# Optimization experiments

Measured on AMD Instinct MI355X. Metric: run time of the kernel, lower is better.

Reference implementation:

```python
import jax, jax.numpy as jnp
import numpy as np

SPATIAL_SHAPES = [(128, 128), (64, 64), (32, 32), (16, 16)]
B, Q, D, NH, NL, NP = 8, 900, 256, 8, 4, 4
S = sum(h * w for h, w in SPATIAL_SHAPES)  # 21760
HD = D // NH


def bilinear_sample(img, x, y):
    # img: (H, W, C); x, y: (Q, P) pixel coords (grid_sample align_corners=False convention)
    H, W, _ = img.shape
    x0 = jnp.floor(x)
    y0 = jnp.floor(y)
    out = 0.0
    for yi in (y0, y0 + 1.0):
        for xi in (x0, x0 + 1.0):
            w = (1.0 - jnp.abs(x - xi)) * (1.0 - jnp.abs(y - yi))
            valid = (xi >= 0) & (xi <= W - 1) & (yi >= 0) & (yi <= H - 1)
            xc = jnp.clip(xi, 0, W - 1).astype(jnp.int32)
            yc = jnp.clip(yi, 0, H - 1).astype(jnp.int32)
            out = out + img[yc, xc] * (w * valid)[..., None]  # (Q, P, C)
    return out


def setup_inputs() -> dict:
    key = jax.random.key(0)
    ks = jax.random.split(key, 10)
    return {
        'hidden_states': jax.random.normal(ks[0], (B, Q, D), jnp.float32),
        'encoder_hidden_states': jax.random.normal(ks[1], (B, S, D), jnp.float32),
        'position_embeddings': jax.random.normal(ks[2], (B, Q, D), jnp.float32),
        'reference_points': jax.random.uniform(ks[3], (B, Q, NL, 2), jnp.float32),
        'spatial_shapes': jnp.array(SPATIAL_SHAPES, jnp.int32),
        'W_value': jax.random.normal(ks[4], (D, D), jnp.float32) * 0.02,
        'b_value': jnp.zeros((D,), jnp.float32),
        'W_off': jax.random.normal(ks[5], (D, NH * NL * NP * 2), jnp.float32) * 0.02,
        'b_off': jnp.zeros((NH * NL * NP * 2,), jnp.float32),
        'W_attn': jax.random.normal(ks[6], (D, NH * NL * NP), jnp.float32) * 0.02,
        'b_attn': jnp.zeros((NH * NL * NP,), jnp.float32),
        'W_out': jax.random.normal(ks[7], (D, D), jnp.float32) * 0.02,
        'b_out': jnp.zeros((D,), jnp.float32),
    }


def reference(hidden_states, encoder_hidden_states, position_embeddings, reference_points,
              spatial_shapes, W_value, b_value, W_off, b_off, W_attn, b_attn, W_out, b_out):
    hs = hidden_states + position_embeddings                      # (B, Q, D)
    value = (encoder_hidden_states @ W_value + b_value).reshape(B, S, NH, HD)
    offsets = (hs @ W_off + b_off).reshape(B, Q, NH, NL, NP, 2)
    attw = jax.nn.softmax((hs @ W_attn + b_attn).reshape(B, Q, NH, NL * NP), -1)
    attw = attw.reshape(B, Q, NH, NL, NP)
    # offset normalizer: (W_l, H_l) per level
    norm = jnp.stack([spatial_shapes[:, 1], spatial_shapes[:, 0]], -1).astype(hs.dtype)
    loc = reference_points[:, :, None, :, None, :] + offsets / norm[None, None, None, :, None, :]
    # loc: (B, Q, NH, NL, NP, 2) in [0, 1]
    out = jnp.zeros((B * NH, Q, HD), hs.dtype)
    start = 0
    for lvl, (Hl, Wl) in enumerate(SPATIAL_SHAPES):
        v = value[:, start:start + Hl * Wl].reshape(B, Hl, Wl, NH, HD)
        v = v.transpose(0, 3, 1, 2, 4).reshape(B * NH, Hl, Wl, HD)
        g = 2.0 * loc[:, :, :, lvl] - 1.0                         # (B, Q, NH, NP, 2)
        x = ((g[..., 0] + 1.0) * 0.5 * Wl - 0.5).transpose(0, 2, 1, 3).reshape(B * NH, Q, NP)
        y = ((g[..., 1] + 1.0) * 0.5 * Hl - 0.5).transpose(0, 2, 1, 3).reshape(B * NH, Q, NP)
        sampled = jax.vmap(bilinear_sample)(v, x, y)              # (B*NH, Q, NP, HD)
        w = attw[:, :, :, lvl].transpose(0, 2, 1, 3).reshape(B * NH, Q, NP)
        out = out + jnp.einsum('nqpd,nqp->nqd', sampled, w)
        start += Hl * Wl
    out = out.reshape(B, NH, Q, HD).transpose(0, 2, 1, 3).reshape(B, Q, D)
    return (out @ W_out + b_out, attw)
```

## Files before the change

### kernel.cpp

```cpp
#include <hip/hip_runtime.h>
#include <hip/hip_bf16.h>

constexpr int Bc  = 8;
constexpr int Qn  = 900;
constexpr int Sn  = 21760;

__constant__ int LVL_W[4]     = {128, 64, 32, 16};
__constant__ int LVL_H[4]     = {128, 64, 32, 16};
__constant__ int LVL_START[4] = {0, 16384, 20480, 21504};

typedef __attribute__((ext_vector_type(8))) short short8;
typedef __attribute__((ext_vector_type(4))) float f32x4;

__device__ __forceinline__ unsigned short f2bf(float x) {
    union { float f; unsigned int u; } z; z.f = x;
    unsigned int r = (z.u + 0x7FFF + ((z.u >> 16) & 1)) >> 16;
    return (unsigned short)r;
}
__device__ __forceinline__ float bf2f(unsigned short u) {
    union { unsigned int i; float f; } z;
    z.i = ((unsigned int)u) << 16;
    return z.f;
}

__global__ __launch_bounds__(256) void wfrag_k(const float* __restrict__ W, int N,
                                               unsigned short* __restrict__ out) {
    int gid = blockIdx.x * 256 + threadIdx.x;
    int frag = gid >> 6, lane = gid & 63;
    int ntile = frag >> 3, s = frag & 7;
    int n = ntile * 16 + (lane & 15);
    int kb = s * 32 + (lane >> 4) * 8;
    unsigned short* o = out + (size_t)gid * 8;
#pragma unroll
    for (int j = 0; j < 8; ++j)
        o[j] = f2bf(W[(size_t)(kb + j) * N + n]);
}

__global__ __launch_bounds__(512) void gemm_value_mfma(const float* __restrict__ A,
                                                       const unsigned short* __restrict__ Wfrag,
                                                       const float* __restrict__ bias,
                                                       unsigned short* __restrict__ C) {
    __shared__ unsigned short As[64 * 256];

    const int t  = threadIdx.x;
    const int bm = blockIdx.x;

    const float4* A4 = reinterpret_cast<const float4*>(A + (size_t)bm * 64 * 256);
#pragma unroll
    for (int i = 0; i < 4; ++i) {
        int c = i * 512 + t;
        int row = c >> 5;
        int kus = (c & 31) * 8;
        float4 v0 = A4[c * 2], v1 = A4[c * 2 + 1];
        union { short8 v; unsigned short u[8]; } pk;
        pk.u[0] = f2bf(v0.x); pk.u[1] = f2bf(v0.y); pk.u[2] = f2bf(v0.z); pk.u[3] = f2bf(v0.w);
        pk.u[4] = f2bf(v1.x); pk.u[5] = f2bf(v1.y); pk.u[6] = f2bf(v1.z); pk.u[7] = f2bf(v1.w);
        int idx = row * 256 + (kus ^ ((row & 7) << 3));
        *reinterpret_cast<short8*>(&As[idx]) = pk.v;
    }

    const int lane = t & 63;
    const int w    = t >> 6;
    const int wr   = w >> 2, wc = w & 3;
    const int lq   = lane >> 4, lr = lane & 15;

    f32x4 acc[2][4];
#pragma unroll
    for (int mt = 0; mt < 2; ++mt)
#pragma unroll
        for (int nt = 0; nt < 4; ++nt) acc[mt][nt] = (f32x4){0.f, 0.f, 0.f, 0.f};

    __syncthreads();

#pragma unroll 2
    for (int s = 0; s < 8; ++s) {
        short8 bfr[4];
#pragma unroll
        for (int nt = 0; nt < 4; ++nt) {
            int ntile = wc * 4 + nt;
            size_t off = ((size_t)((ntile * 8 + s) * 64 + lane)) * 8;
            bfr[nt] = *reinterpret_cast<const short8*>(Wfrag + off);
        }
        const int kus = s * 32 + lq * 8;
#pragma unroll
        for (int mt = 0; mt < 2; ++mt) {
            int r   = wr * 32 + mt * 16 + lr;
            int idx = r * 256 + (kus ^ ((r & 7) << 3));
            short8 a = *reinterpret_cast<const short8*>(&As[idx]);
#pragma unroll
            for (int nt = 0; nt < 4; ++nt)
                acc[mt][nt] = __builtin_amdgcn_mfma_f32_16x16x32_bf16(bfr[nt], a, acc[mt][nt], 0, 0, 0);
        }
    }

#pragma unroll
    for (int nt = 0; nt < 4; ++nt) {
        int n0 = wc * 64 + nt * 16 + lq * 4;
        float4 bb = *reinterpret_cast<const float4*>(&bias[n0]);
#pragma unroll
        for (int mt = 0; mt < 2; ++mt) {
            int row = bm * 64 + wr * 32 + mt * 16 + lr;
            ushort4 o;
            o.x = f2bf(acc[mt][nt][0] + bb.x);
            o.y = f2bf(acc[mt][nt][1] + bb.y);
            o.z = f2bf(acc[mt][nt][2] + bb.z);
            o.w = f2bf(acc[mt][nt][3] + bb.w);
            *reinterpret_cast<ushort4*>(&C[(size_t)row * 256 + n0]) = o;
        }
    }
}

__global__ __launch_bounds__(512) void gemm_qk_mfma(const float* __restrict__ A1,
                                                    const float* __restrict__ A2,
                                                    const unsigned short* __restrict__ WfragQK,
                                                    const float* __restrict__ bo,
                                                    const float* __restrict__ ba,
                                                    float* __restrict__ off_raw,
                                                    float* __restrict__ logits, int M) {
    __shared__ unsigned short As[64 * 256];

    const int t  = threadIdx.x;
    const int bm = blockIdx.x;
    const int maxr = M - bm * 64;

    const float4* A14 = reinterpret_cast<const float4*>(A1 + (size_t)bm * 64 * 256);
    const float4* A24 = reinterpret_cast<const float4*>(A2 + (size_t)bm * 64 * 256);
#pragma unroll
    for (int i = 0; i < 4; ++i) {
        int c = i * 512 + t;
        int row = c >> 5;
        int kus = (c & 31) * 8;
        float4 v0 = make_float4(0.f,0.f,0.f,0.f), v1 = v0;
        if (row < maxr) {
            float4 x0 = A14[c * 2], y0 = A24[c * 2];
            float4 x1 = A14[c * 2 + 1], y1 = A24[c * 2 + 1];
            v0 = make_float4(x0.x + y0.x, x0.y + y0.y, x0.z + y0.z, x0.w + y0.w);
            v1 = make_float4(x1.x + y1.x, x1.y + y1.y, x1.z + y1.z, x1.w + y1.w);
        }
        union { short8 v; unsigned short u[8]; } pk;
        pk.u[0] = f2bf(v0.x); pk.u[1] = f2bf(v0.y); pk.u[2] = f2bf(v0.z); pk.u[3] = f2bf(v0.w);
        pk.u[4] = f2bf(v1.x); pk.u[5] = f2bf(v1.y); pk.u[6] = f2bf(v1.z); pk.u[7] = f2bf(v1.w);
        int idx = row * 256 + (kus ^ ((row & 7) << 3));
        *reinterpret_cast<short8*>(&As[idx]) = pk.v;
    }

    const int lane = t & 63;
    const int w    = t >> 6;
    const int wr   = w >> 2, wc = w & 3;
    const int lq   = lane >> 4, lr = lane & 15;

    f32x4 acc[2][6];
#pragma unroll
    for (int mt = 0; mt < 2; ++mt)
#pragma unroll
        for (int nt = 0; nt < 6; ++nt) acc[mt][nt] = (f32x4){0.f, 0.f, 0.f, 0.f};

    __syncthreads();

#pragma unroll 2
    for (int s = 0; s < 8; ++s) {
        short8 bfr[6];
#pragma unroll
        for (int nt = 0; nt < 6; ++nt) {
            int ntc = wc * 6 + nt;
            const unsigned short* p = (ntc < 16)
                ? WfragQK + ((size_t)(ntc * 8 + s)) * 512
                : WfragQK + 65536 + ((size_t)((ntc - 16) * 8 + s)) * 512;
            bfr[nt] = *reinterpret_cast<const short8*>(p + lane * 8);
        }
        const int kus = s * 32 + lq * 8;
#pragma unroll
        for (int mt = 0; mt < 2; ++mt) {
            int r   = wr * 32 + mt * 16 + lr;
            int idx = r * 256 + (kus ^ ((r & 7) << 3));
            short8 a = *reinterpret_cast<const short8*>(&As[idx]);
#pragma unroll
            for (int nt = 0; nt < 6; ++nt)
                acc[mt][nt] = __builtin_amdgcn_mfma_f32_16x16x32_bf16(bfr[nt], a, acc[mt][nt], 0, 0, 0);
        }
    }

#pragma unroll
    for (int nt = 0; nt < 6; ++nt) {
        int ntc = wc * 6 + nt;
        float* base; int stride, n0;
        float4 bb;
        if (ntc < 16) { n0 = ntc * 16 + lq * 4;        base = off_raw; stride = 256;
                        bb = *reinterpret_cast<const float4*>(&bo[n0]); }
        else          { n0 = (ntc - 16) * 16 + lq * 4; base = logits;  stride = 128;
                        bb = *reinterpret_cast<const float4*>(&ba[n0]); }
#pragma unroll
        for (int mt = 0; mt < 2; ++mt) {
            int r = wr * 32 + mt * 16 + lr;
            if (r < maxr) {
                int row = bm * 64 + r;
                float4 o = make_float4(acc[mt][nt][0] + bb.x, acc[mt][nt][1] + bb.y,
                                       acc[mt][nt][2] + bb.z, acc[mt][nt][3] + bb.w);
                *reinterpret_cast<float4*>(&base[(size_t)row * stride + n0]) = o;
            }
        }
    }
}

__global__ __launch_bounds__(512) void gemm_out_mfma(const float* __restrict__ A,
                                                     const unsigned short* __restrict__ Wfrag,
                                                     const float* __restrict__ bias,
                                                     float* __restrict__ C, int M) {
    __shared__ unsigned short As[64 * 256];

    const int t  = threadIdx.x;
    const int bm = blockIdx.x;
    const int maxr = M - bm * 64;

    const float4* A4 = reinterpret_cast<const float4*>(A + (size_t)bm * 64 * 256);
#pragma unroll
    for (int i = 0; i < 4; ++i) {
        int c = i * 512 + t;
        int row = c >> 5;
        int kus = (c & 31) * 8;
        float4 v0 = make_float4(0.f,0.f,0.f,0.f), v1 = v0;
        if (row < maxr) { v0 = A4[c * 2]; v1 = A4[c * 2 + 1]; }
        union { short8 v; unsigned short u[8]; } pk;
        pk.u[0] = f2bf(v0.x); pk.u[1] = f2bf(v0.y); pk.u[2] = f2bf(v0.z); pk.u[3] = f2bf(v0.w);
        pk.u[4] = f2bf(v1.x); pk.u[5] = f2bf(v1.y); pk.u[6] = f2bf(v1.z); pk.u[7] = f2bf(v1.w);
        int idx = row * 256 + (kus ^ ((row & 7) << 3));
        *reinterpret_cast<short8*>(&As[idx]) = pk.v;
    }

    const int lane = t & 63;
    const int w    = t >> 6;
    const int wr   = w >> 2, wc = w & 3;
    const int lq   = lane >> 4, lr = lane & 15;

    f32x4 acc[2][4];
#pragma unroll
    for (int mt = 0; mt < 2; ++mt)
#pragma unroll
        for (int nt = 0; nt < 4; ++nt) acc[mt][nt] = (f32x4){0.f, 0.f, 0.f, 0.f};

    __syncthreads();

#pragma unroll 2
    for (int s = 0; s < 8; ++s) {
        short8 bfr[4];
#pragma unroll
        for (int nt = 0; nt < 4; ++nt) {
            int ntile = wc * 4 + nt;
            size_t off = ((size_t)((ntile * 8 + s) * 64 + lane)) * 8;
            bfr[nt] = *reinterpret_cast<const short8*>(Wfrag + off);
        }
        const int kus = s * 32 + lq * 8;
#pragma unroll
        for (int mt = 0; mt < 2; ++mt) {
            int r   = wr * 32 + mt * 16 + lr;
            int idx = r * 256 + (kus ^ ((r & 7) << 3));
            short8 a = *reinterpret_cast<const short8*>(&As[idx]);
#pragma unroll
            for (int nt = 0; nt < 4; ++nt)
                acc[mt][nt] = __builtin_amdgcn_mfma_f32_16x16x32_bf16(bfr[nt], a, acc[mt][nt], 0, 0, 0);
        }
    }

#pragma unroll
    for (int nt = 0; nt < 4; ++nt) {
        int n0 = wc * 64 + nt * 16 + lq * 4;
        float4 bb = *reinterpret_cast<const float4*>(&bias[n0]);
#pragma unroll
        for (int mt = 0; mt < 2; ++mt) {
            int r = wr * 32 + mt * 16 + lr;
            if (r < maxr) {
                int row = bm * 64 + r;
                float4 o = make_float4(acc[mt][nt][0] + bb.x, acc[mt][nt][1] + bb.y,
                                       acc[mt][nt][2] + bb.z, acc[mt][nt][3] + bb.w);
                *reinterpret_cast<float4*>(&C[(size_t)row * 256 + n0]) = o;
            }
        }
    }
}

__global__ __launch_bounds__(256) void softmax_k(const float* __restrict__ logits,
                                                 float* __restrict__ attw) {
    int tid = blockIdx.x * 256 + threadIdx.x;
    const float4* in = reinterpret_cast<const float4*>(logits + (size_t)tid * 16);
    float v[16];
    float4 a0 = in[0], a1 = in[1], a2 = in[2], a3 = in[3];
    v[0]=a0.x; v[1]=a0.y; v[2]=a0.z; v[3]=a0.w;
    v[4]=a1.x; v[5]=a1.y; v[6]=a1.z; v[7]=a1.w;
    v[8]=a2.x; v[9]=a2.y; v[10]=a2.z; v[11]=a2.w;
    v[12]=a3.x; v[13]=a3.y; v[14]=a3.z; v[15]=a3.w;
    float m = v[0];
#pragma unroll
    for (int i = 1; i < 16; ++i) m = fmaxf(m, v[i]);
    float s = 0.f;
#pragma unroll
    for (int i = 0; i < 16; ++i) { v[i] = __expf(v[i] - m); s += v[i]; }
    float inv = 1.f / s;
    float4* o = reinterpret_cast<float4*>(attw + (size_t)tid * 16);
    o[0] = make_float4(v[0]*inv, v[1]*inv, v[2]*inv, v[3]*inv);
    o[1] = make_float4(v[4]*inv, v[5]*inv, v[6]*inv, v[7]*inv);
    o[2] = make_float4(v[8]*inv, v[9]*inv, v[10]*inv, v[11]*inv);
    o[3] = make_float4(v[12]*inv, v[13]*inv, v[14]*inv, v[15]*inv);
}

__global__ __launch_bounds__(256) void sample_k(const unsigned short* __restrict__ value,
                                                const float* __restrict__ off_raw,
                                                const float* __restrict__ refp,
                                                const float* __restrict__ attw,
                                                float* __restrict__ out_pre) {
    const int lane = threadIdx.x & 7;
    const int g    = threadIdx.x >> 3;
    const int idx  = blockIdx.x * 32 + g;
    const int h    = idx & 7;
    const int bq   = idx >> 3;
    const int b    = bq / Qn;

    const ushort4* v4 = reinterpret_cast<const ushort4*>(value);
    const size_t vbase4 = (size_t)b * (Sn * 64) + h * 8 + lane;

    const float* offs = off_raw + (size_t)bq * 256 + h * 32;
    const float* aw   = attw    + (size_t)bq * 128 + h * 16;
    const float* rp   = refp    + (size_t)bq * 8;

    float acc0 = 0.f, acc1 = 0.f, acc2 = 0.f, acc3 = 0.f;

#pragma unroll
    for (int lvl = 0; lvl < 4; ++lvl) {
        const int Wl = LVL_W[lvl], Hl = LVL_H[lvl];
        const float fW = (float)Wl, fH = (float)Hl;
        const float rx = rp[lvl * 2 + 0], ry = rp[lvl * 2 + 1];
        const size_t lb4 = vbase4 + (size_t)LVL_START[lvl] * 64;
#pragma unroll
        for (int p = 0; p < 4; ++p) {
            const float w  = aw[lvl * 4 + p];
            const float locx = rx + offs[lvl * 8 + p * 2 + 0] / fW;
            const float locy = ry + offs[lvl * 8 + p * 2 + 1] / fH;
            const float x = locx * fW - 0.5f;
            const float y = locy * fH - 0.5f;
            const float x0f = floorf(x), y0f = floorf(y);
            const int x0 = (int)x0f, y0 = (int)y0f;
            const int x1 = x0 + 1, y1 = y0 + 1;
            const float fx = x - x0f, fy = y - y0f;
            const float vx0 = (x0 >= 0 && x0 < Wl) ? 1.f : 0.f;
            const float vx1 = (x1 >= 0 && x1 < Wl) ? 1.f : 0.f;
            const float vy0 = (y0 >= 0 && y0 < Hl) ? 1.f : 0.f;
            const float vy1 = (y1 >= 0 && y1 < Hl) ? 1.f : 0.f;
            const int xc0 = min(max(x0, 0), Wl - 1);
            const int xc1 = min(max(x1, 0), Wl - 1);
            const int yc0 = min(max(y0, 0), Hl - 1);
            const int yc1 = min(max(y1, 0), Hl - 1);
            const float w00 = w * (1.f - fx) * (1.f - fy) * vx0 * vy0;
            const float w01 = w * fx         * (1.f - fy) * vx1 * vy0;
            const float w10 = w * (1.f - fx) * fy         * vx0 * vy1;
            const float w11 = w * fx         * fy         * vx1 * vy1;

            const ushort4 t00 = v4[lb4 + (size_t)(yc0 * Wl + xc0) * 64];
            const ushort4 t01 = v4[lb4 + (size_t)(yc0 * Wl + xc1) * 64];
            const ushort4 t10 = v4[lb4 + (size_t)(yc1 * Wl + xc0) * 64];
            const ushort4 t11 = v4[lb4 + (size_t)(yc1 * Wl + xc1) * 64];

            acc0 += w00 * bf2f(t00.x) + w01 * bf2f(t01.x) + w10 * bf2f(t10.x) + w11 * bf2f(t11.x);
            acc1 += w00 * bf2f(t00.y) + w01 * bf2f(t01.y) + w10 * bf2f(t10.y) + w11 * bf2f(t11.y);
            acc2 += w00 * bf2f(t00.z) + w01 * bf2f(t01.z) + w10 * bf2f(t10.z) + w11 * bf2f(t11.z);
            acc3 += w00 * bf2f(t00.w) + w01 * bf2f(t01.w) + w10 * bf2f(t10.w) + w11 * bf2f(t11.w);
        }
    }
    reinterpret_cast<float4*>(out_pre)[(size_t)bq * 64 + h * 8 + lane] =
        make_float4(acc0, acc1, acc2, acc3);
}

extern "C" void kernel_launch(void* const* d_in, const int* in_sizes, int n_in,
                              void* d_out, int out_size, void* d_ws, size_t ws_size,
                              hipStream_t stream) {
    const float* hidden = (const float*)d_in[0];
    const float* ehs    = (const float*)d_in[1];
    const float* pos    = (const float*)d_in[2];
    const float* refp   = (const float*)d_in[3];
    const float* Wv   = (const float*)d_in[5];
    const float* bv   = (const float*)d_in[6];
    const float* Wo   = (const float*)d_in[7];
    const float* bo   = (const float*)d_in[8];
    const float* Wa   = (const float*)d_in[9];
    const float* ba   = (const float*)d_in[10];
    const float* Wout = (const float*)d_in[11];
    const float* bout = (const float*)d_in[12];

    float* ws = (float*)d_ws;
    unsigned short* WfragQK = (unsigned short*)ws;
    unsigned short* WfragO  = (unsigned short*)(ws + 49152);
    float* off_raw = ws + 1843200;
    float* logits  = ws + 3686400;
    float* out_pre = ws + 4608000;
    unsigned short* value = (unsigned short*)(ws + 6451200);
    unsigned short* WfragV = (unsigned short*)out_pre;

    float* outv = (float*)d_out;
    float* attw = outv + 1843200;

    wfrag_k<<<32, 256, 0, stream>>>(Wv,   256, WfragV);
    wfrag_k<<<32, 256, 0, stream>>>(Wout, 256, WfragO);
    wfrag_k<<<32, 256, 0, stream>>>(Wo,   256, WfragQK);
    wfrag_k<<<16, 256, 0, stream>>>(Wa,   128, WfragQK + 65536);
    gemm_value_mfma<<<2720, 512, 0, stream>>>(ehs, WfragV, bv, value);
    gemm_qk_mfma<<<113, 512, 0, stream>>>(hidden, pos, WfragQK, bo, ba, off_raw, logits, Bc * Qn);
    softmax_k<<<225, 256, 0, stream>>>(logits, attw);
    sample_k<<<1800, 256, 0, stream>>>(value, off_raw, refp, attw, out_pre);
    gemm_out_mfma<<<113, 512, 0, stream>>>(out_pre, WfragO, bout, outv, Bc * Qn);
}
```

Baseline: 149.1 us.

## Make value GEMM persistent over four row tiles with double-buffered LDS prefetch

The value projection GEMM now gives each block four consecutive 64-row tiles instead of one, and launches a quarter as many blocks. While the MFMAs for the current tile run, the fp32 A rows for the next tile are loaded into registers, then converted to bf16 and written into a second LDS buffer. Bias loads and swizzle indices are hoisted out of the tile loop. The aim is to hide global-load latency and amortise the per-block setup. In exchange the kernel uses twice the LDS and more registers, which may lower occupancy, and 680 blocks may not fill the GPU evenly.

```diff
diff --git a/kernel.cpp b/kernel.cpp
--- a/kernel.cpp
+++ b/kernel.cpp
@@ -40,72 +40,110 @@
                                                        const unsigned short* __restrict__ Wfrag,
                                                        const float* __restrict__ bias,
                                                        unsigned short* __restrict__ C) {
-    __shared__ unsigned short As[64 * 256];
-
-    const int t  = threadIdx.x;
-    const int bm = blockIdx.x;
-
-    const float4* A4 = reinterpret_cast<const float4*>(A + (size_t)bm * 64 * 256);
+    __shared__ unsigned short As[2 * 16384];
+
+    const int t    = threadIdx.x;
+    const int blk  = blockIdx.x;
+    const int lane = t & 63;
+    const int w    = t >> 6;
+    const int wr   = w >> 2, wc = w & 3;
+    const int lq   = lane >> 4, lr = lane & 15;
+
+    int sidx[4];
 #pragma unroll
     for (int i = 0; i < 4; ++i) {
         int c = i * 512 + t;
         int row = c >> 5;
         int kus = (c & 31) * 8;
-        float4 v0 = A4[c * 2], v1 = A4[c * 2 + 1];
-        union { short8 v; unsigned short u[8]; } pk;
-        pk.u[0] = f2bf(v0.x); pk.u[1] = f2bf(v0.y); pk.u[2] = f2bf(v0.z); pk.u[3] = f2bf(v0.w);
-        pk.u[4] = f2bf(v1.x); pk.u[5] = f2bf(v1.y); pk.u[6] = f2bf(v1.z); pk.u[7] = f2bf(v1.w);
-        int idx = row * 256 + (kus ^ ((row & 7) << 3));
-        *reinterpret_cast<short8*>(&As[idx]) = pk.v;
-    }
-
-    const int lane = t & 63;
-    const int w    = t >> 6;
-    const int wr   = w >> 2, wc = w & 3;
-    const int lq   = lane >> 4, lr = lane & 15;
-
-    f32x4 acc[2][4];
-#pragma unroll
-    for (int mt = 0; mt < 2; ++mt)
-#pragma unroll
-        for (int nt = 0; nt < 4; ++nt) acc[mt][nt] = (f32x4){0.f, 0.f, 0.f, 0.f};
-
+        sidx[i] = row * 256 + (kus ^ ((row & 7) << 3));
+    }
+
+    const float4* A4 = reinterpret_cast<const float4*>(A);
+    float4 ld[4][2];
+
+    auto stage_load = [&](int bm) {
+        const float4* src = A4 + (size_t)bm * 4096;
+#pragma unroll
+        for (int i = 0; i < 4; ++i) {
+            int c = i * 512 + t;
+            ld[i][0] = src[c * 2];
+            ld[i][1] = src[c * 2 + 1];
+        }
+    };
+    auto stage_write = [&](int bufsel) {
+        unsigned short* buf = &As[bufsel * 16384];
+#pragma unroll
+        for (int i = 0; i < 4; ++i) {
+            union { short8 v; unsigned short u[8]; } pk;
+            pk.u[0] = f2bf(ld[i][0].x); pk.u[1] = f2bf(ld[i][0].y);
+            pk.u[2] = f2bf(ld[i][0].z); pk.u[3] = f2bf(ld[i][0].w);
+            pk.u[4] = f2bf(ld[i][1].x); pk.u[5] = f2bf(ld[i][1].y);
+            pk.u[6] = f2bf(ld[i][1].z); pk.u[7] = f2bf(ld[i][1].w);
+            *reinterpret_cast<short8*>(&buf[sidx[i]]) = pk.v;
+        }
+    };
+
+    float4 bb[4];
+#pragma unroll
+    for (int nt = 0; nt < 4; ++nt)
+        bb[nt] = *reinterpret_cast<const float4*>(&bias[wc * 64 + nt * 16 + lq * 4]);
+
+    const int bm0 = blk * 4;
+    stage_load(bm0);
+    stage_write(0);
     __syncthreads();
 
+#pragma unroll 1
+    for (int tt = 0; tt < 4; ++tt) {
+        if (tt < 3) stage_load(bm0 + tt + 1);
+
+        const unsigned short* buf = &As[(tt & 1) * 16384];
+        f32x4 acc[2][4];
+#pragma unroll
+        for (int mt = 0; mt < 2; ++mt)
+#pragma unroll
+            for (int nt = 0; nt < 4; ++nt) acc[mt][nt] = (f32x4){0.f, 0.f, 0.f, 0.f};
+
 #pragma unroll 2
-    for (int s = 0; s < 8; ++s) {
-        short8 bfr[4];
+        for (int s = 0; s < 8; ++s) {
+            short8 bfr[4];
+#pragma unroll
+            for (int nt = 0; nt < 4; ++nt) {
+                int ntile = wc * 4 + nt;
+                size_t off = ((size_t)((ntile * 8 + s) * 64 + lane)) * 8;
+                bfr[nt] = *reinterpret_cast<const short8*>(Wfrag + off);
+            }
+            const int kus = s * 32 + lq * 8;
+#pragma unroll
+            for (int mt = 0; mt < 2; ++mt) {
+                int r   = wr * 32 + mt * 16 + lr;
+                int idx = r * 256 + (kus ^ ((r & 7) << 3));
+                short8 a = *reinterpret_cast<const short8*>(&buf[idx]);
+#pragma unroll
+                for (int nt = 0; nt < 4; ++nt)
+                    acc[mt][nt] = __builtin_amdgcn_mfma_f32_16x16x32_bf16(bfr[nt], a, acc[mt][nt], 0, 0, 0);
+            }
+        }
+
+        const int bm = bm0 + tt;
 #pragma unroll
         for (int nt = 0; nt < 4; ++nt) {
-            int ntile = wc * 4 + nt;
-            size_t off = ((size_t)((ntile * 8 + s) * 64 + lane)) * 8;
-            bfr[nt] = *reinterpret_cast<const short8*>(Wfrag + off);
-        }
-        const int kus = s * 32 + lq * 8;
-#pragma unroll
-        for (int mt = 0; mt < 2; ++mt) {
-            int r   = wr * 32 + mt * 16 + lr;
-            int idx = r * 256 + (kus ^ ((r & 7) << 3));
-            short8 a = *reinterpret_cast<const short8*>(&As[idx]);
-#pragma unroll
-            for (int nt = 0; nt < 4; ++nt)
-                acc[mt][nt] = __builtin_amdgcn_mfma_f32_16x16x32_bf16(bfr[nt], a, acc[mt][nt], 0, 0, 0);
-        }
-    }
-
-#pragma unroll
-    for (int nt = 0; nt < 4; ++nt) {
-        int n0 = wc * 64 + nt * 16 + lq * 4;
-        float4 bb = *reinterpret_cast<const float4*>(&bias[n0]);
-#pragma unroll
-        for (int mt = 0; mt < 2; ++mt) {
-            int row = bm * 64 + wr * 32 + mt * 16 + lr;
-            ushort4 o;
-            o.x = f2bf(acc[mt][nt][0] + bb.x);
-            o.y = f2bf(acc[mt][nt][1] + bb.y);
-            o.z = f2bf(acc[mt][nt][2] + bb.z);
-            o.w = f2bf(acc[mt][nt][3] + bb.w);
-            *reinterpret_cast<ushort4*>(&C[(size_t)row * 256 + n0]) = o;
+            int n0 = wc * 64 + nt * 16 + lq * 4;
+#pragma unroll
+            for (int mt = 0; mt < 2; ++mt) {
+                int row = bm * 64 + wr * 32 + mt * 16 + lr;
+                ushort4 o;
+                o.x = f2bf(acc[mt][nt][0] + bb[nt].x);
+                o.y = f2bf(acc[mt][nt][1] + bb[nt].y);
+                o.z = f2bf(acc[mt][nt][2] + bb[nt].z);
+                o.w = f2bf(acc[mt][nt][3] + bb[nt].w);
+                *reinterpret_cast<ushort4*>(&C[(size_t)row * 256 + n0]) = o;
+            }
+        }
+
+        if (tt < 3) {
+            stage_write((tt + 1) & 1);
+            __syncthreads();
         }
     }
 }
@@ -400,7 +438,7 @@
     wfrag_k<<<32, 256, 0, stream>>>(Wout, 256, WfragO);
     wfrag_k<<<32, 256, 0, stream>>>(Wo,   256, WfragQK);
     wfrag_k<<<16, 256, 0, stream>>>(Wa,   128, WfragQK + 65536);
-    gemm_value_mfma<<<2720, 512, 0, stream>>>(ehs, WfragV, bv, value);
+    gemm_value_mfma<<<680, 512, 0, stream>>>(ehs, WfragV, bv, value);
     gemm_qk_mfma<<<113, 512, 0, stream>>>(hidden, pos, WfragQK, bo, ba, off_raw, logits, Bc * Qn);
     softmax_k<<<225, 256, 0, stream>>>(logits, attw);
     sample_k<<<1800, 256, 0, stream>>>(value, off_raw, refp, attw, out_pre);
```

New measurement: 152.2 us. +2.1%, slower.

## Merge value and query GEMMs into one launch; fuse softmax into sampling

Applied to the files above, without the earlier changes.

The value-projection GEMM and the offset/attention-logit GEMM now run in a single launch, with blocks branching on their index. The softmax kernel is removed: each sampling group recomputes the softmax of its 16 logits and writes attw. Sampling splits the four levels across two half-groups of lanes and combines them with a shuffle, doubling thread count per head. This cuts two launches and an attw round-trip, but every lane repeats the softmax and the merged GEMM kernel may use more registers.

```diff
diff --git a/kernel.cpp b/kernel.cpp
--- a/kernel.cpp
+++ b/kernel.cpp
@@ -5,8 +5,6 @@
 constexpr int Qn  = 900;
 constexpr int Sn  = 21760;
 
-__constant__ int LVL_W[4]     = {128, 64, 32, 16};
-__constant__ int LVL_H[4]     = {128, 64, 32, 16};
 __constant__ int LVL_START[4] = {0, 16384, 20480, 21504};
 
 typedef __attribute__((ext_vector_type(8))) short short8;
@@ -36,167 +34,155 @@
         o[j] = f2bf(W[(size_t)(kb + j) * N + n]);
 }
 
-__global__ __launch_bounds__(512) void gemm_value_mfma(const float* __restrict__ A,
-                                                       const unsigned short* __restrict__ Wfrag,
-                                                       const float* __restrict__ bias,
-                                                       unsigned short* __restrict__ C) {
+__global__ __launch_bounds__(512) void uber_gemm(
+        const float* __restrict__ Aehs, const unsigned short* __restrict__ WfragV,
+        const float* __restrict__ bv, unsigned short* __restrict__ Cval,
+        const float* __restrict__ A1, const float* __restrict__ A2,
+        const unsigned short* __restrict__ WfragQK,
+        const float* __restrict__ bo, const float* __restrict__ ba,
+        float* __restrict__ off_raw, float* __restrict__ logits, int Mqk) {
     __shared__ unsigned short As[64 * 256];
 
-    const int t  = threadIdx.x;
-    const int bm = blockIdx.x;
-
-    const float4* A4 = reinterpret_cast<const float4*>(A + (size_t)bm * 64 * 256);
-#pragma unroll
-    for (int i = 0; i < 4; ++i) {
-        int c = i * 512 + t;
-        int row = c >> 5;
-        int kus = (c & 31) * 8;
-        float4 v0 = A4[c * 2], v1 = A4[c * 2 + 1];
-        union { short8 v; unsigned short u[8]; } pk;
-        pk.u[0] = f2bf(v0.x); pk.u[1] = f2bf(v0.y); pk.u[2] = f2bf(v0.z); pk.u[3] = f2bf(v0.w);
-        pk.u[4] = f2bf(v1.x); pk.u[5] = f2bf(v1.y); pk.u[6] = f2bf(v1.z); pk.u[7] = f2bf(v1.w);
-        int idx = row * 256 + (kus ^ ((row & 7) << 3));
-        *reinterpret_cast<short8*>(&As[idx]) = pk.v;
-    }
-
+    const int t    = threadIdx.x;
     const int lane = t & 63;
     const int w    = t >> 6;
     const int wr   = w >> 2, wc = w & 3;
     const int lq   = lane >> 4, lr = lane & 15;
 
-    f32x4 acc[2][4];
-#pragma unroll
-    for (int mt = 0; mt < 2; ++mt)
-#pragma unroll
-        for (int nt = 0; nt < 4; ++nt) acc[mt][nt] = (f32x4){0.f, 0.f, 0.f, 0.f};
-
-    __syncthreads();
+    if (blockIdx.x < 2720) {
+        const int bm = blockIdx.x;
+        const float4* A4 = reinterpret_cast<const float4*>(Aehs + (size_t)bm * 64 * 256);
+#pragma unroll
+        for (int i = 0; i < 4; ++i) {
+            int c = i * 512 + t;
+            int row = c >> 5;
+            int kus = (c & 31) * 8;
+            float4 v0 = A4[c * 2], v1 = A4[c * 2 + 1];
+            union { short8 v; unsigned short u[8]; } pk;
+            pk.u[0] = f2bf(v0.x); pk.u[1] = f2bf(v0.y); pk.u[2] = f2bf(v0.z); pk.u[3] = f2bf(v0.w);
+            pk.u[4] = f2bf(v1.x); pk.u[5] = f2bf(v1.y); pk.u[6] = f2bf(v1.z); pk.u[7] = f2bf(v1.w);
+            int idx = row * 256 + (kus ^ ((row & 7) << 3));
+            *reinterpret_cast<short8*>(&As[idx]) = pk.v;
+        }
+
+        f32x4 acc[2][4];
+#pragma unroll
+        for (int mt = 0; mt < 2; ++mt)
+#pragma unroll
+            for (int nt = 0; nt < 4; ++nt) acc[mt][nt] = (f32x4){0.f, 0.f, 0.f, 0.f};
+
+        __syncthreads();
 
 #pragma unroll 2
-    for (int s = 0; s < 8; ++s) {
-        short8 bfr[4];
+        for (int s = 0; s < 8; ++s) {
+            short8 bfr[4];
+#pragma unroll
+            for (int nt = 0; nt < 4; ++nt) {
+                int ntile = wc * 4 + nt;
+                size_t off = ((size_t)((ntile * 8 + s) * 64 + lane)) * 8;
+                bfr[nt] = *reinterpret_cast<const short8*>(WfragV + off);
+            }
+            const int kus = s * 32 + lq * 8;
+#pragma unroll
+            for (int mt = 0; mt < 2; ++mt) {
+                int r   = wr * 32 + mt * 16 + lr;
+                int idx = r * 256 + (kus ^ ((r & 7) << 3));
+                short8 a = *reinterpret_cast<const short8*>(&As[idx]);
+#pragma unroll
+                for (int nt = 0; nt < 4; ++nt)
+                    acc[mt][nt] = __builtin_amdgcn_mfma_f32_16x16x32_bf16(bfr[nt], a, acc[mt][nt], 0, 0, 0);
+            }
+        }
+
 #pragma unroll
         for (int nt = 0; nt < 4; ++nt) {
-            int ntile = wc * 4 + nt;
-            size_t off = ((size_t)((ntile * 8 + s) * 64 + lane)) * 8;
-            bfr[nt] = *reinterpret_cast<const short8*>(Wfrag + off);
-        }
-        const int kus = s * 32 + lq * 8;
-#pragma unroll
-        for (int mt = 0; mt < 2; ++mt) {
-            int r   = wr * 32 + mt * 16 + lr;
-            int idx = r * 256 + (kus ^ ((r & 7) << 3));
-            short8 a = *reinterpret_cast<const short8*>(&As[idx]);
-#pragma unroll
-            for (int nt = 0; nt < 4; ++nt)
-                acc[mt][nt] = __builtin_amdgcn_mfma_f32_16x16x32_bf16(bfr[nt], a, acc[mt][nt], 0, 0, 0);
-        }
-    }
-
-#pragma unroll
-    for (int nt = 0; nt < 4; ++nt) {
-        int n0 = wc * 64 + nt * 16 + lq * 4;
-        float4 bb = *reinterpret_cast<const float4*>(&bias[n0]);
-#pragma unroll
-        for (int mt = 0; mt < 2; ++mt) {
-            int row = bm * 64 + wr * 32 + mt * 16 + lr;
-            ushort4 o;
-            o.x = f2bf(acc[mt][nt][0] + bb.x);
-            o.y = f2bf(acc[mt][nt][1] + bb.y);
-            o.z = f2bf(acc[mt][nt][2] + bb.z);
-            o.w = f2bf(acc[mt][nt][3] + bb.w);
-            *reinterpret_cast<ushort4*>(&C[(size_t)row * 256 + n0]) = o;
-        }
-    }
-}
-
-__global__ __launch_bounds__(512) void gemm_qk_mfma(const float* __restrict__ A1,
-                                                    const float* __restrict__ A2,
-                                                    const unsigned short* __restrict__ WfragQK,
-                                                    const float* __restrict__ bo,
-                                                    const float* __restrict__ ba,
-                                                    float* __restrict__ off_raw,
-                                                    float* __restrict__ logits, int M) {
-    __shared__ unsigned short As[64 * 256];
-
-    const int t  = threadIdx.x;
-    const int bm = blockIdx.x;
-    const int maxr = M - bm * 64;
-
-    const float4* A14 = reinterpret_cast<const float4*>(A1 + (size_t)bm * 64 * 256);
-    const float4* A24 = reinterpret_cast<const float4*>(A2 + (size_t)bm * 64 * 256);
-#pragma unroll
-    for (int i = 0; i < 4; ++i) {
-        int c = i * 512 + t;
-        int row = c >> 5;
-        int kus = (c & 31) * 8;
-        float4 v0 = make_float4(0.f,0.f,0.f,0.f), v1 = v0;
-        if (row < maxr) {
-            float4 x0 = A14[c * 2], y0 = A24[c * 2];
-            float4 x1 = A14[c * 2 + 1], y1 = A24[c * 2 + 1];
-            v0 = make_float4(x0.x + y0.x, x0.y + y0.y, x0.z + y0.z, x0.w + y0.w);
-            v1 = make_float4(x1.x + y1.x, x1.y + y1.y, x1.z + y1.z, x1.w + y1.w);
-        }
-        union { short8 v; unsigned short u[8]; } pk;
-        pk.u[0] = f2bf(v0.x); pk.u[1] = f2bf(v0.y); pk.u[2] = f2bf(v0.z); pk.u[3] = f2bf(v0.w);
-        pk.u[4] = f2bf(v1.x); pk.u[5] = f2bf(v1.y); pk.u[6] = f2bf(v1.z); pk.u[7] = f2bf(v1.w);
-        int idx = row * 256 + (kus ^ ((row & 7) << 3));
-        *reinterpret_cast<short8*>(&As[idx]) = pk.v;
-    }
-
-    const int lane = t & 63;
-    const int w    = t >> 6;
-    const int wr   = w >> 2, wc = w & 3;
-    const int lq   = lane >> 4, lr = lane & 15;
-
-    f32x4 acc[2][6];
-#pragma unroll
-    for (int mt = 0; mt < 2; ++mt)
-#pragma unroll
-        for (int nt = 0; nt < 6; ++nt) acc[mt][nt] = (f32x4){0.f, 0.f, 0.f, 0.f};
-
-    __syncthreads();
+            int n0 = wc * 64 + nt * 16 + lq * 4;
+            float4 bb = *reinterpret_cast<const float4*>(&bv[n0]);
+#pragma unroll
+            for (int mt = 0; mt < 2; ++mt) {
+                int row = bm * 64 + wr * 32 + mt * 16 + lr;
+                ushort4 o;
+                o.x = f2bf(acc[mt][nt][0] + bb.x);
+                o.y = f2bf(acc[mt][nt][1] + bb.y);
+                o.z = f2bf(acc[mt][nt][2] + bb.z);
+                o.w = f2bf(acc[mt][nt][3] + bb.w);
+                *reinterpret_cast<ushort4*>(&Cval[(size_t)row * 256 + n0]) = o;
+            }
+        }
+    } else {
+        const int bm = blockIdx.x - 2720;
+        const int maxr = Mqk - bm * 64;
+
+        const float4* A14 = reinterpret_cast<const float4*>(A1 + (size_t)bm * 64 * 256);
+        const float4* A24 = reinterpret_cast<const float4*>(A2 + (size_t)bm * 64 * 256);
+#pragma unroll
+        for (int i = 0; i < 4; ++i) {
+            int c = i * 512 + t;
+            int row = c >> 5;
+            int kus = (c & 31) * 8;
+            float4 v0 = make_float4(0.f,0.f,0.f,0.f), v1 = v0;
+            if (row < maxr) {
+                float4 x0 = A14[c * 2], y0 = A24[c * 2];
+                float4 x1 = A14[c * 2 + 1], y1 = A24[c * 2 + 1];
+                v0 = make_float4(x0.x + y0.x, x0.y + y0.y, x0.z + y0.z, x0.w + y0.w);
+                v1 = make_float4(x1.x + y1.x, x1.y + y1.y, x1.z + y1.z, x1.w + y1.w);
+            }
+            union { short8 v; unsigned short u[8]; } pk;
+            pk.u[0] = f2bf(v0.x); pk.u[1] = f2bf(v0.y); pk.u[2] = f2bf(v0.z); pk.u[3] = f2bf(v0.w);
+            pk.u[4] = f2bf(v1.x); pk.u[5] = f2bf(v1.y); pk.u[6] = f2bf(v1.z); pk.u[7] = f2bf(v1.w);
+            int idx = row * 256 + (kus ^ ((row & 7) << 3));
+            *reinterpret_cast<short8*>(&As[idx]) = pk.v;
+        }
+
+        f32x4 acc[2][6];
+#pragma unroll
+        for (int mt = 0; mt < 2; ++mt)
+#pragma unroll
+            for (int nt = 0; nt < 6; ++nt) acc[mt][nt] = (f32x4){0.f, 0.f, 0.f, 0.f};
+
+        __syncthreads();
 
 #pragma unroll 2
-    for (int s = 0; s < 8; ++s) {
-        short8 bfr[6];
+        for (int s = 0; s < 8; ++s) {
+            short8 bfr[6];
+#pragma unroll
+            for (int nt = 0; nt < 6; ++nt) {
+                int ntc = wc * 6 + nt;
+                const unsigned short* p = (ntc < 16)
+                    ? WfragQK + ((size_t)(ntc * 8 + s)) * 512
+                    : WfragQK + 65536 + ((size_t)((ntc - 16) * 8 + s)) * 512;
+                bfr[nt] = *reinterpret_cast<const short8*>(p + lane * 8);
+            }
+            const int kus = s * 32 + lq * 8;
+#pragma unroll
+            for (int mt = 0; mt < 2; ++mt) {
+                int r   = wr * 32 + mt * 16 + lr;
+                int idx = r * 256 + (kus ^ ((r & 7) << 3));
+                short8 a = *reinterpret_cast<const short8*>(&As[idx]);
+#pragma unroll
+                for (int nt = 0; nt < 6; ++nt)
+                    acc[mt][nt] = __builtin_amdgcn_mfma_f32_16x16x32_bf16(bfr[nt], a, acc[mt][nt], 0, 0, 0);
+            }
+        }
+
 #pragma unroll
         for (int nt = 0; nt < 6; ++nt) {
             int ntc = wc * 6 + nt;
-            const unsigned short* p = (ntc < 16)
-                ? WfragQK + ((size_t)(ntc * 8 + s)) * 512
-                : WfragQK + 65536 + ((size_t)((ntc - 16) * 8 + s)) * 512;
-            bfr[nt] = *reinterpret_cast<const short8*>(p + lane * 8);
-        }
-        const int kus = s * 32 + lq * 8;
-#pragma unroll
-        for (int mt = 0; mt < 2; ++mt) {
-            int r   = wr * 32 + mt * 16 + lr;
-            int idx = r * 256 + (kus ^ ((r & 7) << 3));
-            short8 a = *reinterpret_cast<const short8*>(&As[idx]);
-#pragma unroll
-            for (int nt = 0; nt < 6; ++nt)
-                acc[mt][nt] = __builtin_amdgcn_mfma_f32_16x16x32_bf16(bfr[nt], a, acc[mt][nt], 0, 0, 0);
-        }
-    }
-
-#pragma unroll
-    for (int nt = 0; nt < 6; ++nt) {
-        int ntc = wc * 6 + nt;
-        float* base; int stride, n0;
-        float4 bb;
-        if (ntc < 16) { n0 = ntc * 16 + lq * 4;        base = off_raw; stride = 256;
-                        bb = *reinterpret_cast<const float4*>(&bo[n0]); }
-        else          { n0 = (ntc - 16) * 16 + lq * 4; base = logits;  stride = 128;
-                        bb = *reinterpret_cast<const float4*>(&ba[n0]); }
-#pragma unroll
-        for (int mt = 0; mt < 2; ++mt) {
-            int r = wr * 32 + mt * 16 + lr;
-            if (r < maxr) {
-                int row = bm * 64 + r;
-                float4 o = make_float4(acc[mt][nt][0] + bb.x, acc[mt][nt][1] + bb.y,
-                                       acc[mt][nt][2] + bb.z, acc[mt][nt][3] + bb.w);
-                *reinterpret_cast<float4*>(&base[(size_t)row * stride + n0]) = o;
+            float* base; int stride, n0;
+            float4 bb;
+            if (ntc < 16) { n0 = ntc * 16 + lq * 4;        base = off_raw; stride = 256;
+                            bb = *reinterpret_cast<const float4*>(&bo[n0]); }
+            else          { n0 = (ntc - 16) * 16 + lq * 4; base = logits;  stride = 128;
+                            bb = *reinterpret_cast<const float4*>(&ba[n0]); }
+#pragma unroll
+            for (int mt = 0; mt < 2; ++mt) {
+                int r = wr * 32 + mt * 16 + lr;
+                if (r < maxr) {
+                    int row = bm * 64 + r;
+                    float4 o = make_float4(acc[mt][nt][0] + bb.x, acc[mt][nt][1] + bb.y,
+                                           acc[mt][nt][2] + bb.z, acc[mt][nt][3] + bb.w);
+                    *reinterpret_cast<float4*>(&base[(size_t)row * stride + n0]) = o;
+                }
             }
         }
     }
@@ -278,12 +264,24 @@
     }
 }
 
-__global__ __launch_bounds__(256) void softmax_k(const float* __restrict__ logits,
-                                                 float* __restrict__ attw) {
-    int tid = blockIdx.x * 256 + threadIdx.x;
-    const float4* in = reinterpret_cast<const float4*>(logits + (size_t)tid * 16);
+__global__ __launch_bounds__(256) void sample_fused_k(const unsigned short* __restrict__ value,
+                                                      const float* __restrict__ off_raw,
+                                                      const float* __restrict__ refp,
+                                                      const float* __restrict__ logits,
+                                                      float* __restrict__ attw,
+                                                      float* __restrict__ out_pre) {
+    const int L    = threadIdx.x & 15;
+    const int g    = threadIdx.x >> 4;
+    const int idx  = blockIdx.x * 16 + g;
+    const int h    = idx & 7;
+    const int bq   = idx >> 3;
+    const int b    = bq / Qn;
+    const int ch   = L & 7;
+    const int pq   = L >> 3;
+
+    const float4* lg = reinterpret_cast<const float4*>(logits + (size_t)idx * 16);
     float v[16];
-    float4 a0 = in[0], a1 = in[1], a2 = in[2], a3 = in[3];
+    float4 a0 = lg[0], a1 = lg[1], a2 = lg[2], a3 = lg[3];
     v[0]=a0.x; v[1]=a0.y; v[2]=a0.z; v[3]=a0.w;
     v[4]=a1.x; v[5]=a1.y; v[6]=a1.z; v[7]=a1.w;
     v[8]=a2.x; v[9]=a2.y; v[10]=a2.z; v[11]=a2.w;
@@ -295,43 +293,39 @@
 #pragma unroll
     for (int i = 0; i < 16; ++i) { v[i] = __expf(v[i] - m); s += v[i]; }
     float inv = 1.f / s;
-    float4* o = reinterpret_cast<float4*>(attw + (size_t)tid * 16);
-    o[0] = make_float4(v[0]*inv, v[1]*inv, v[2]*inv, v[3]*inv);
-    o[1] = make_float4(v[4]*inv, v[5]*inv, v[6]*inv, v[7]*inv);
-    o[2] = make_float4(v[8]*inv, v[9]*inv, v[10]*inv, v[11]*inv);
-    o[3] = make_float4(v[12]*inv, v[13]*inv, v[14]*inv, v[15]*inv);
-}
-
-__global__ __launch_bounds__(256) void sample_k(const unsigned short* __restrict__ value,
-                                                const float* __restrict__ off_raw,
-                                                const float* __restrict__ refp,
-                                                const float* __restrict__ attw,
-                                                float* __restrict__ out_pre) {
-    const int lane = threadIdx.x & 7;
-    const int g    = threadIdx.x >> 3;
-    const int idx  = blockIdx.x * 32 + g;
-    const int h    = idx & 7;
-    const int bq   = idx >> 3;
-    const int b    = bq / Qn;
+#pragma unroll
+    for (int i = 0; i < 16; ++i) v[i] *= inv;
+
+    if (pq == 0 && ch < 4) {
+        float4 o;
+        if      (ch == 0) o = make_float4(v[0],  v[1],  v[2],  v[3]);
+        else if (ch == 1) o = make_float4(v[4],  v[5],  v[6],  v[7]);
+        else if (ch == 2) o = make_float4(v[8],  v[9],  v[10], v[11]);
+        else              o = make_float4(v[12], v[13], v[14], v[15]);
+        reinterpret_cast<float4*>(attw + (size_t)idx * 16)[ch] = o;
+    }
+
+    float w8[8];
+#pragma unroll
+    for (int i = 0; i < 8; ++i) w8[i] = (pq == 0) ? v[i] : v[i + 8];
 
     const ushort4* v4 = reinterpret_cast<const ushort4*>(value);
-    const size_t vbase4 = (size_t)b * (Sn * 64) + h * 8 + lane;
-
+    const size_t vbase4 = (size_t)b * (Sn * 64) + h * 8 + ch;
     const float* offs = off_raw + (size_t)bq * 256 + h * 32;
-    const float* aw   = attw    + (size_t)bq * 128 + h * 16;
     const float* rp   = refp    + (size_t)bq * 8;
 
     float acc0 = 0.f, acc1 = 0.f, acc2 = 0.f, acc3 = 0.f;
 
 #pragma unroll
-    for (int lvl = 0; lvl < 4; ++lvl) {
-        const int Wl = LVL_W[lvl], Hl = LVL_H[lvl];
+    for (int li = 0; li < 2; ++li) {
+        const int lvl = pq * 2 + li;
+        const int Wl = 128 >> lvl, Hl = 128 >> lvl;
         const float fW = (float)Wl, fH = (float)Hl;
         const float rx = rp[lvl * 2 + 0], ry = rp[lvl * 2 + 1];
         const size_t lb4 = vbase4 + (size_t)LVL_START[lvl] * 64;
 #pragma unroll
         for (int p = 0; p < 4; ++p) {
-            const float w  = aw[lvl * 4 + p];
+            const float w  = w8[li * 4 + p];
             const float locx = rx + offs[lvl * 8 + p * 2 + 0] / fW;
             const float locy = ry + offs[lvl * 8 + p * 2 + 1] / fH;
             const float x = locx * fW - 0.5f;
@@ -364,8 +358,15 @@
             acc3 += w00 * bf2f(t00.w) + w01 * bf2f(t01.w) + w10 * bf2f(t10.w) + w11 * bf2f(t11.w);
         }
     }
-    reinterpret_cast<float4*>(out_pre)[(size_t)bq * 64 + h * 8 + lane] =
-        make_float4(acc0, acc1, acc2, acc3);
+
+    acc0 += __shfl_xor(acc0, 8);
+    acc1 += __shfl_xor(acc1, 8);
+    acc2 += __shfl_xor(acc2, 8);
+    acc3 += __shfl_xor(acc3, 8);
+
+    if (pq == 0)
+        reinterpret_cast<float4*>(out_pre)[(size_t)bq * 64 + h * 8 + ch] =
+            make_float4(acc0, acc1, acc2, acc3);
 }
 
 extern "C" void kernel_launch(void* const* d_in, const int* in_sizes, int n_in,
@@ -400,9 +401,9 @@
     wfrag_k<<<32, 256, 0, stream>>>(Wout, 256, WfragO);
     wfrag_k<<<32, 256, 0, stream>>>(Wo,   256, WfragQK);
     wfrag_k<<<16, 256, 0, stream>>>(Wa,   128, WfragQK + 65536);
-    gemm_value_mfma<<<2720, 512, 0, stream>>>(ehs, WfragV, bv, value);
-    gemm_qk_mfma<<<113, 512, 0, stream>>>(hidden, pos, WfragQK, bo, ba, off_raw, logits, Bc * Qn);
-    softmax_k<<<225, 256, 0, stream>>>(logits, attw);
-    sample_k<<<1800, 256, 0, stream>>>(value, off_raw, refp, attw, out_pre);
+    uber_gemm<<<2833, 512, 0, stream>>>(ehs, WfragV, bv, value,
+                                        hidden, pos, WfragQK, bo, ba,
+                                        off_raw, logits, Bc * Qn);
+    sample_fused_k<<<3600, 256, 0, stream>>>(value, off_raw, refp, logits, attw, out_pre);
     gemm_out_mfma<<<113, 512, 0, stream>>>(out_pre, WfragO, bout, outv, Bc * Qn);
 }
```

Result: no change. 147.5 us (-1.1%).
